# Optimization experiments

Measured on AMD Instinct MI355X. Metric: run time of the kernel, lower is better.

## Reference

```python
import jax, jax.numpy as jnp
import numpy as np

D_MODEL = 1024
NUM_HEADS = 16
D_K = D_MODEL // NUM_HEADS


def setup_inputs() -> dict:
    key = jax.random.key(0)
    k1, k2, k3 = jax.random.split(key, 3)
    x = jax.random.normal(k1, (2, 2048, D_MODEL), dtype=jnp.float32)
    # torch Linear(d, 3d): weight shape [3d, d], y = x @ W.T
    W_QKV = jax.random.normal(k2, (3 * D_MODEL, D_MODEL), dtype=jnp.float32) * (1.0 / np.sqrt(D_MODEL))
    W_O = jax.random.normal(k3, (D_MODEL, D_MODEL), dtype=jnp.float32) * (1.0 / np.sqrt(D_MODEL))
    return {"x": x, "W_QKV": W_QKV, "W_O": W_O}


def reference(x, W_QKV, W_O):
    B, T, C = x.shape
    qkv = jnp.einsum('btc,fc->btf', x, W_QKV)  # [B,T,3C]
    q, k, v = jnp.split(qkv, 3, axis=-1)
    def heads(t):
        return t.reshape(B, T, NUM_HEADS, D_K).transpose(0, 2, 1, 3)  # [B,H,T,Dk]
    Q, K, V = heads(q), heads(k), heads(v)
    scores = jnp.einsum('bhqd,bhkd->bhqk', Q, K) / jnp.sqrt(jnp.float32(D_K))
    causal = jnp.tril(jnp.ones((T, T), dtype=bool))
    scores = jnp.where(causal, scores, -jnp.inf)
    attn = jax.nn.softmax(scores, axis=-1)
    out = jnp.einsum('bhqk,bhkd->bhqd', attn, V)
    out = out.transpose(0, 2, 1, 3).reshape(B, T, C)
    return jnp.einsum('btc,oc->bto', out, W_O)
```

## Files before the change

kernel.cpp:

```cpp
#include <hip/hip_runtime.h>
#include <hip/hip_bf16.h>
#include <stdint.h>
#include <stddef.h>


typedef __attribute__((ext_vector_type(8)))  __bf16   bf16x8;
typedef __attribute__((ext_vector_type(4)))  float    f32x4;
typedef __attribute__((ext_vector_type(16))) float    f32x16;
typedef __attribute__((ext_vector_type(4)))  uint32_t u32x4;

#define AS1(p) ((__attribute__((address_space(1))) void*)(p))
#define AS3(p) ((__attribute__((address_space(3))) void*)(p))

static constexpr int Tq    = 2048;
static constexpr int Cd    = 1024;
static constexpr int Mrows = 2 * Tq;

#define QSCALE 0.18033688011112042f

__global__ __launch_bounds__(256) void cvt_bf16_kernel(const float* __restrict__ in,
                                                       __bf16* __restrict__ out, int n8)
{
    int idx    = blockIdx.x * blockDim.x + threadIdx.x;
    int stride = gridDim.x * blockDim.x;
    for (int i = idx; i < n8; i += stride) {
        f32x4 a = ((const f32x4*)in)[i * 2 + 0];
        f32x4 b = ((const f32x4*)in)[i * 2 + 1];
        bf16x8 o;
#pragma unroll
        for (int j = 0; j < 4; ++j) { o[j] = (__bf16)a[j]; o[4 + j] = (__bf16)b[j]; }
        ((bf16x8*)out)[i] = o;
    }
}

__global__ __launch_bounds__(256) void transpose_v_kernel(const __bf16* __restrict__ qkv,
                                                          __bf16* __restrict__ vT)
{
    __shared__ __bf16 tile[64][65];
    const int t   = threadIdx.x;
    const int r0  = blockIdx.x * 64;
    const int hd0 = blockIdx.y * 64;

    {
        const int rr = t >> 2, c16 = (t & 3) * 16;
        const __bf16* src = qkv + (size_t)(r0 + rr) * 3072 + 2048 + hd0 + c16;
        bf16x8 a = *(const bf16x8*)(src);
        bf16x8 b = *(const bf16x8*)(src + 8);
#pragma unroll
        for (int j = 0; j < 8; ++j) { tile[rr][c16 + j] = a[j]; tile[rr][c16 + 8 + j] = b[j]; }
    }
    __syncthreads();
    {
        const int hd_loc = t >> 2, rg = (t & 3) * 16;
        bf16x8 a, b;
#pragma unroll
        for (int j = 0; j < 8; ++j) { a[j] = tile[rg + j][hd_loc]; b[j] = tile[rg + 8 + j][hd_loc]; }
        __bf16* dst = vT + (size_t)(hd0 + hd_loc) * Mrows + r0 + rg;
        *(bf16x8*)(dst)     = a;
        *(bf16x8*)(dst + 8) = b;
    }
}

template <bool OUT_BF16>
__global__ __launch_bounds__(256) void gemm_bt_kernel(const __bf16* __restrict__ A,
                                                      const __bf16* __restrict__ Bm,
                                                      float* __restrict__ Cf,
                                                      __bf16* __restrict__ Cb,
                                                      int N, int K, int qcols, float qscale)
{
    __shared__ __align__(16) __bf16 As[128 * 64];
    __shared__ __align__(16) __bf16 Bs[128 * 64];

    const int tid = threadIdx.x;
    const int l   = tid & 63;
    const int w   = tid >> 6;
    const int wr  = w >> 1, wc = w & 1;
    const int lo  = l & 15, hi = l >> 4;
    const int m0  = blockIdx.x * 128;
    const int n0  = blockIdx.y * 128;

    f32x4 acc[4][4] = {};

    for (int kk = 0; kk < K; kk += 64) {
#pragma unroll
        for (int i = 0; i < 4; ++i) {
            int s   = i * 256 + tid;
            int row = s >> 3;
            int gg  = (s & 7) ^ (row & 7);
            const __bf16* srcA = A  + (size_t)(m0 + row) * K + kk + gg * 8;
            const __bf16* srcB = Bm + (size_t)(n0 + row) * K + kk + gg * 8;
            __builtin_amdgcn_global_load_lds(AS1(srcA), AS3((char*)As + s * 16), 16, 0, 0);
            __builtin_amdgcn_global_load_lds(AS1(srcB), AS3((char*)Bs + s * 16), 16, 0, 0);
        }
        __syncthreads();

#pragma unroll
        for (int ks = 0; ks < 2; ++ks) {
            bf16x8 af[4], bfr[4];
#pragma unroll
            for (int m = 0; m < 4; ++m) {
                int row = wr * 64 + m * 16 + lo;
                int gl  = (ks * 4 + hi) ^ (row & 7);
                af[m] = *(const bf16x8*)((const char*)As + row * 128 + gl * 16);
            }
#pragma unroll
            for (int n = 0; n < 4; ++n) {
                int row = wc * 64 + n * 16 + lo;
                int gl  = (ks * 4 + hi) ^ (row & 7);
                bfr[n] = *(const bf16x8*)((const char*)Bs + row * 128 + gl * 16);
            }
#pragma unroll
            for (int m = 0; m < 4; ++m)
#pragma unroll
                for (int n = 0; n < 4; ++n)
                    acc[m][n] = __builtin_amdgcn_mfma_f32_16x16x32_bf16(af[m], bfr[n], acc[m][n], 0, 0, 0);
        }
        __syncthreads();
    }

#pragma unroll
    for (int m = 0; m < 4; ++m)
#pragma unroll
        for (int n = 0; n < 4; ++n)
#pragma unroll
            for (int r = 0; r < 4; ++r) {
                int row = m0 + wr * 64 + m * 16 + hi * 4 + r;
                int col = n0 + wc * 64 + n * 16 + lo;
                float v = acc[m][n][r];
                if (col < qcols) v *= qscale;
                if (OUT_BF16) Cb[(size_t)row * N + col] = (__bf16)v;
                else          Cf[(size_t)row * N + col] = v;
            }
}

__global__ __launch_bounds__(128) void attn_kernel(const __bf16* __restrict__ qkv,
                                                   const __bf16* __restrict__ vT,
                                                   __bf16* __restrict__ att)
{
    __shared__ __align__(16) __bf16 Ks[2][64 * 64];
    __shared__ __align__(16) __bf16 Vs[2][64 * 64];

    const int tid = threadIdx.x;
    const int l   = tid & 63;
    const int w   = tid >> 6;
    const int lo5 = l & 31, hi5 = l >> 5;

    const int bid = blockIdx.x;
    const int g   = (bid >> 5) & 7;
    const int c   = bid >> 8;
    const int qt  = (c & 1) ? (16 - ((c >> 1) << 4) + g)
                            : (31 - ((c >> 1) << 4) - g);
    const int bh  = bid & 31;
    const int h   = bh & 15;
    const int b   = bh >> 4;

    const __bf16* Kbase = qkv + (size_t)b * Tq * 3072 + 1024 + h * 64;
    const __bf16* Vbase = vT  + (size_t)h * 64 * Mrows + b * Tq;

    const int qb0 = qt * 64;
    const int nt  = qt + 1;

    bf16x8 onesf;
#pragma unroll
    for (int jj = 0; jj < 8; ++jj) onesf[jj] = (__bf16)1.0f;

    bf16x8 qf[4];
    {
        const __bf16* Qp = qkv + (size_t)(b * Tq + qb0 + w * 32 + lo5) * 3072 + h * 64 + hi5 * 8;
#pragma unroll
        for (int ds = 0; ds < 4; ++ds) qf[ds] = *(const bf16x8*)(Qp + ds * 16);
    }

    f32x16 o0 = {}, o1 = {}, ls = {};
    float m = -1e30f;

#pragma unroll
    for (int i = 0; i < 4; ++i) {
        int s = i * 128 + tid;
        int row = s >> 3, gg = (s & 7) ^ (row & 7);
        __builtin_amdgcn_global_load_lds(AS1(Kbase + (size_t)row * 3072 + gg * 8),
                                         AS3((char*)Ks[0] + s * 16), 16, 0, 0);
        __builtin_amdgcn_global_load_lds(AS1(Vbase + (size_t)row * Mrows + gg * 8),
                                         AS3((char*)Vs[0] + s * 16), 16, 0, 0);
    }
    __syncthreads();

    int cur = 0;
    for (int t = 0; t < nt; ++t) {
        if (t + 1 < nt) {
            const int kn = (t + 1) * 64;
#pragma unroll
            for (int i = 0; i < 4; ++i) {
                int s = i * 128 + tid;
                int row = s >> 3, gg = (s & 7) ^ (row & 7);
                __builtin_amdgcn_global_load_lds(AS1(Kbase + (size_t)(kn + row) * 3072 + gg * 8),
                                                 AS3((char*)Ks[cur ^ 1] + s * 16), 16, 0, 0);
                __builtin_amdgcn_global_load_lds(AS1(Vbase + (size_t)row * Mrows + kn + gg * 8),
                                                 AS3((char*)Vs[cur ^ 1] + s * 16), 16, 0, 0);
            }
        }

        f32x16 sf0 = {}, sf1 = {};
        __builtin_amdgcn_s_setprio(1);
#pragma unroll
        for (int ds = 0; ds < 4; ++ds) {
            {
                int row = lo5;
                int gl  = (ds * 2 + hi5) ^ (row & 7);
                bf16x8 kf = *(const bf16x8*)((const char*)Ks[cur] + row * 128 + gl * 16);
                sf0 = __builtin_amdgcn_mfma_f32_32x32x16_bf16(kf, qf[ds], sf0, 0, 0, 0);
            }
            {
                int row = 32 + lo5;
                int gl  = (ds * 2 + hi5) ^ (row & 7);
                bf16x8 kf = *(const bf16x8*)((const char*)Ks[cur] + row * 128 + gl * 16);
                sf1 = __builtin_amdgcn_mfma_f32_32x32x16_bf16(kf, qf[ds], sf1, 0, 0, 0);
            }
        }
        __builtin_amdgcn_s_setprio(0);

        if (t == qt) {
            const int ql = w * 32 + lo5;
#pragma unroll
            for (int r = 0; r < 16; ++r) {
                int kc = (r & 3) + 8 * (r >> 2) + 4 * hi5;
                if (kc      > ql) sf0[r] = -1e30f;
                if (kc + 32 > ql) sf1[r] = -1e30f;
            }
        }

        float t0 = fmaxf(sf0[0],  fmaxf(sf0[1],  sf0[2]));
        float t1 = fmaxf(sf0[3],  fmaxf(sf0[4],  sf0[5]));
        float t2 = fmaxf(sf0[6],  fmaxf(sf0[7],  sf0[8]));
        float t3 = fmaxf(sf0[9],  fmaxf(sf0[10], sf0[11]));
        float t4 = fmaxf(sf0[12], fmaxf(sf0[13], sf0[14]));
        float t5 = fmaxf(sf1[0],  fmaxf(sf1[1],  sf1[2]));
        float t6 = fmaxf(sf1[3],  fmaxf(sf1[4],  sf1[5]));
        float t7 = fmaxf(sf1[6],  fmaxf(sf1[7],  sf1[8]));
        float t8 = fmaxf(sf1[9],  fmaxf(sf1[10], sf1[11]));
        float t9 = fmaxf(sf1[12], fmaxf(sf1[13], sf1[14]));
        float u0 = fmaxf(t0, fmaxf(t1, t2));
        float u1 = fmaxf(t3, fmaxf(t4, sf0[15]));
        float u2 = fmaxf(t5, fmaxf(t6, t7));
        float u3 = fmaxf(t8, fmaxf(t9, sf1[15]));
        float pmh = fmaxf(fmaxf(u0, u1), fmaxf(u2, u3));
        float pm  = fmaxf(pmh, __shfl_xor(pmh, 32));

        if (__any(pm > m + 8.0f)) {
            float mnew = fmaxf(m, pm);
            float fac  = __builtin_amdgcn_exp2f(m - mnew);
            m = mnew;
#pragma unroll
            for (int r = 0; r < 16; ++r) {
                int qreg = (r & 3) + 8 * (r >> 2) + 4 * hi5;
                float fr = __shfl(fac, qreg);
                o0[r] *= fr;
                o1[r] *= fr;
                ls[r] *= fr;
            }
        }

        __builtin_amdgcn_s_setprio(1);
#pragma unroll
        for (int kb = 0; kb < 2; ++kb) {
            uint32_t W[8];
#pragma unroll
            for (int wd = 0; wd < 8; ++wd) {
                float sa = (kb == 0) ? sf0[2 * wd]     : sf1[2 * wd];
                float sb = (kb == 0) ? sf0[2 * wd + 1] : sf1[2 * wd + 1];
                __bf16 ba = (__bf16)__builtin_amdgcn_exp2f(sa - m);
                __bf16 bb = (__bf16)__builtin_amdgcn_exp2f(sb - m);
                W[wd] = (uint32_t)__builtin_bit_cast(uint16_t, ba)
                      | ((uint32_t)__builtin_bit_cast(uint16_t, bb) << 16);
            }
            uint32_t Za = __shfl_xor(hi5 ? W[0] : W[2], 32);
            uint32_t Zb = __shfl_xor(hi5 ? W[1] : W[3], 32);
            uint32_t Zc = __shfl_xor(hi5 ? W[4] : W[6], 32);
            uint32_t Zd = __shfl_xor(hi5 ? W[5] : W[7], 32);

            {
                u32x4 fw = { hi5 ? Za : W[0], hi5 ? Zb : W[1],
                             hi5 ? W[2] : Za, hi5 ? W[3] : Zb };
                bf16x8 pa = __builtin_bit_cast(bf16x8, fw);
                const int kstep = kb * 2;
                {
                    int row = lo5;
                    int gl  = (kstep * 2 + hi5) ^ (row & 7);
                    bf16x8 vb = *(const bf16x8*)((const char*)Vs[cur] + row * 128 + gl * 16);
                    o0 = __builtin_amdgcn_mfma_f32_32x32x16_bf16(pa, vb, o0, 0, 0, 0);
                }
                {
                    int row = 32 + lo5;
                    int gl  = (kstep * 2 + hi5) ^ (row & 7);
                    bf16x8 vb = *(const bf16x8*)((const char*)Vs[cur] + row * 128 + gl * 16);
                    o1 = __builtin_amdgcn_mfma_f32_32x32x16_bf16(pa, vb, o1, 0, 0, 0);
                }
                ls = __builtin_amdgcn_mfma_f32_32x32x16_bf16(pa, onesf, ls, 0, 0, 0);
            }
            {
                u32x4 fw = { hi5 ? Zc : W[4], hi5 ? Zd : W[5],
                             hi5 ? W[6] : Zc, hi5 ? W[7] : Zd };
                bf16x8 pa = __builtin_bit_cast(bf16x8, fw);
                const int kstep = kb * 2 + 1;
                {
                    int row = lo5;
                    int gl  = (kstep * 2 + hi5) ^ (row & 7);
                    bf16x8 vb = *(const bf16x8*)((const char*)Vs[cur] + row * 128 + gl * 16);
                    o0 = __builtin_amdgcn_mfma_f32_32x32x16_bf16(pa, vb, o0, 0, 0, 0);
                }
                {
                    int row = 32 + lo5;
                    int gl  = (kstep * 2 + hi5) ^ (row & 7);
                    bf16x8 vb = *(const bf16x8*)((const char*)Vs[cur] + row * 128 + gl * 16);
                    o1 = __builtin_amdgcn_mfma_f32_32x32x16_bf16(pa, vb, o1, 0, 0, 0);
                }
                ls = __builtin_amdgcn_mfma_f32_32x32x16_bf16(pa, onesf, ls, 0, 0, 0);
            }
        }
        __builtin_amdgcn_s_setprio(0);

        __syncthreads();
        cur ^= 1;
    }

#pragma unroll
    for (int r = 0; r < 16; ++r) {
        float lr   = __builtin_amdgcn_rcpf(ls[r]);
        int   qreg = (r & 3) + 8 * (r >> 2) + 4 * hi5;
        int   rowg = b * Tq + qb0 + w * 32 + qreg;
        att[(size_t)rowg * Cd + h * 64 + lo5]      = (__bf16)(o0[r] * lr);
        att[(size_t)rowg * Cd + h * 64 + 32 + lo5] = (__bf16)(o1[r] * lr);
    }
}

extern "C" void kernel_launch(void* const* d_in, const int* in_sizes, int n_in,
                              void* d_out, int out_size, void* d_ws, size_t ws_size,
                              hipStream_t stream)
{
    (void)in_sizes; (void)n_in; (void)out_size; (void)ws_size;

    const float* x    = (const float*)d_in[0];
    const float* Wqkv = (const float*)d_in[1];
    const float* Wo   = (const float*)d_in[2];
    float*       out  = (float*)d_out;

    char* ws = (char*)d_ws;
    __bf16* xb    = (__bf16*)(ws);
    __bf16* wqkvb = (__bf16*)(ws + (size_t)8  * 1024 * 1024);
    __bf16* wob   = (__bf16*)(ws + (size_t)14 * 1024 * 1024);
    __bf16* qkvb  = (__bf16*)(ws + (size_t)16 * 1024 * 1024);
    __bf16* attb  = (__bf16*)(ws + (size_t)40 * 1024 * 1024);
    __bf16* vTb   = xb;

    cvt_bf16_kernel<<<2048, 256, 0, stream>>>(x,    xb,    Mrows * Cd / 8);
    cvt_bf16_kernel<<<1536, 256, 0, stream>>>(Wqkv, wqkvb, 3 * Cd * Cd / 8);
    cvt_bf16_kernel<<<512,  256, 0, stream>>>(Wo,   wob,   Cd * Cd / 8);

    dim3 g1(Mrows / 128, 3 * Cd / 128);
    gemm_bt_kernel<true><<<g1, 256, 0, stream>>>(xb, wqkvb, nullptr, qkvb, 3 * Cd, Cd,
                                                 1024, QSCALE);

    dim3 gt(Mrows / 64, Cd / 64);
    transpose_v_kernel<<<gt, 256, 0, stream>>>(qkvb, vTb);

    attn_kernel<<<1024, 128, 0, stream>>>(qkvb, vTb, attb);

    dim3 g2(Mrows / 128, Cd / 128);
    gemm_bt_kernel<false><<<g2, 256, 0, stream>>>(attb, wob, out, nullptr, Cd, Cd,
                                                  0, 1.0f);
}
```

Measured before the change: 206.2 us.

## Split long causal attention rows into KV chunks with a merge kernel

Query tiles 16-31, which have the longest causal KV ranges, are split into two KV chunks processed by separate blocks. Each chunk writes its unnormalized partial output and its running max and sum to scratch, reusing the output buffer and the freed weight buffer. A new merge kernel combines the two partials. Short tiles still go straight to the output. This targets load imbalance in the tail of the attention grid, at the cost of an extra launch and fp32 partial traffic.

```diff
diff --git a/kernel.cpp b/kernel.cpp
--- a/kernel.cpp
+++ b/kernel.cpp
@@ -133,10 +133,19 @@
             }
 }
 
-__global__ __launch_bounds__(128) void attn_kernel(const __bf16* __restrict__ qkv,
-                                                   const __bf16* __restrict__ vT,
-                                                   __bf16* __restrict__ att)
-{
+__global__ __launch_bounds__(128) void attn_chunk_kernel(const __bf16* __restrict__ qkv,
+                                                         const __bf16* __restrict__ vT,
+                                                         __bf16* __restrict__ att,
+                                                         float* __restrict__ pO,
+                                                         float* __restrict__ stats)
+{
+    constexpr uint8_t QT[48] = {16,17,18,19,20,21,22,23,24,25,26,27,28,29,30,31,
+                                15,31,14,30,13,29,12,28,11,27,10,26, 9,25, 8,24,
+                                 7,23, 6,22, 5,21, 4,20, 3,19, 2,18, 1,17, 0,16};
+    constexpr uint8_t CC[48] = {0,0,0,0,0,0,0,0,0,0,0,0,0,0,0,0,
+                                255,1,255,1,255,1,255,1,255,1,255,1,255,1,255,1,
+                                255,1,255,1,255,1,255,1,255,1,255,1,255,1,255,1};
+
     __shared__ __align__(16) __bf16 Ks[2][64 * 64];
     __shared__ __align__(16) __bf16 Vs[2][64 * 64];
 
@@ -146,19 +155,20 @@
     const int lo5 = l & 31, hi5 = l >> 5;
 
     const int bid = blockIdx.x;
-    const int g   = (bid >> 5) & 7;
-    const int c   = bid >> 8;
-    const int qt  = (c & 1) ? (16 - ((c >> 1) << 4) + g)
-                            : (31 - ((c >> 1) << 4) - g);
+    const int ord = bid >> 5;
     const int bh  = bid & 31;
     const int h   = bh & 15;
     const int b   = bh >> 4;
 
+    const int  qt     = QT[ord];
+    const int  cc     = CC[ord];
+    const bool direct = (cc == 255);
+    const int  t0     = direct ? 0 : cc * 16;
+    const int  t1     = direct ? qt + 1 : min(cc * 16 + 16, qt + 1);
+    const int  qb0    = qt * 64;
+
     const __bf16* Kbase = qkv + (size_t)b * Tq * 3072 + 1024 + h * 64;
     const __bf16* Vbase = vT  + (size_t)h * 64 * Mrows + b * Tq;
-
-    const int qb0 = qt * 64;
-    const int nt  = qt + 1;
 
     bf16x8 onesf;
 #pragma unroll
@@ -178,16 +188,16 @@
     for (int i = 0; i < 4; ++i) {
         int s = i * 128 + tid;
         int row = s >> 3, gg = (s & 7) ^ (row & 7);
-        __builtin_amdgcn_global_load_lds(AS1(Kbase + (size_t)row * 3072 + gg * 8),
+        __builtin_amdgcn_global_load_lds(AS1(Kbase + (size_t)(t0 * 64 + row) * 3072 + gg * 8),
                                          AS3((char*)Ks[0] + s * 16), 16, 0, 0);
-        __builtin_amdgcn_global_load_lds(AS1(Vbase + (size_t)row * Mrows + gg * 8),
+        __builtin_amdgcn_global_load_lds(AS1(Vbase + (size_t)row * Mrows + t0 * 64 + gg * 8),
                                          AS3((char*)Vs[0] + s * 16), 16, 0, 0);
     }
     __syncthreads();
 
     int cur = 0;
-    for (int t = 0; t < nt; ++t) {
-        if (t + 1 < nt) {
+    for (int t = t0; t < t1; ++t) {
+        if (t + 1 < t1) {
             const int kn = (t + 1) * 64;
 #pragma unroll
             for (int i = 0; i < 4; ++i) {
@@ -229,20 +239,20 @@
             }
         }
 
-        float t0 = fmaxf(sf0[0],  fmaxf(sf0[1],  sf0[2]));
-        float t1 = fmaxf(sf0[3],  fmaxf(sf0[4],  sf0[5]));
-        float t2 = fmaxf(sf0[6],  fmaxf(sf0[7],  sf0[8]));
-        float t3 = fmaxf(sf0[9],  fmaxf(sf0[10], sf0[11]));
-        float t4 = fmaxf(sf0[12], fmaxf(sf0[13], sf0[14]));
-        float t5 = fmaxf(sf1[0],  fmaxf(sf1[1],  sf1[2]));
-        float t6 = fmaxf(sf1[3],  fmaxf(sf1[4],  sf1[5]));
-        float t7 = fmaxf(sf1[6],  fmaxf(sf1[7],  sf1[8]));
-        float t8 = fmaxf(sf1[9],  fmaxf(sf1[10], sf1[11]));
-        float t9 = fmaxf(sf1[12], fmaxf(sf1[13], sf1[14]));
-        float u0 = fmaxf(t0, fmaxf(t1, t2));
-        float u1 = fmaxf(t3, fmaxf(t4, sf0[15]));
-        float u2 = fmaxf(t5, fmaxf(t6, t7));
-        float u3 = fmaxf(t8, fmaxf(t9, sf1[15]));
+        float t0m = fmaxf(sf0[0],  fmaxf(sf0[1],  sf0[2]));
+        float t1m = fmaxf(sf0[3],  fmaxf(sf0[4],  sf0[5]));
+        float t2m = fmaxf(sf0[6],  fmaxf(sf0[7],  sf0[8]));
+        float t3m = fmaxf(sf0[9],  fmaxf(sf0[10], sf0[11]));
+        float t4m = fmaxf(sf0[12], fmaxf(sf0[13], sf0[14]));
+        float t5m = fmaxf(sf1[0],  fmaxf(sf1[1],  sf1[2]));
+        float t6m = fmaxf(sf1[3],  fmaxf(sf1[4],  sf1[5]));
+        float t7m = fmaxf(sf1[6],  fmaxf(sf1[7],  sf1[8]));
+        float t8m = fmaxf(sf1[9],  fmaxf(sf1[10], sf1[11]));
+        float t9m = fmaxf(sf1[12], fmaxf(sf1[13], sf1[14]));
+        float u0 = fmaxf(t0m, fmaxf(t1m, t2m));
+        float u1 = fmaxf(t3m, fmaxf(t4m, sf0[15]));
+        float u2 = fmaxf(t5m, fmaxf(t6m, t7m));
+        float u3 = fmaxf(t8m, fmaxf(t9m, sf1[15]));
         float pmh = fmaxf(fmaxf(u0, u1), fmaxf(u2, u3));
         float pm  = fmaxf(pmh, __shfl_xor(pmh, 32));
 
@@ -323,14 +333,75 @@
         cur ^= 1;
     }
 
-#pragma unroll
-    for (int r = 0; r < 16; ++r) {
-        float lr   = __builtin_amdgcn_rcpf(ls[r]);
-        int   qreg = (r & 3) + 8 * (r >> 2) + 4 * hi5;
-        int   rowg = b * Tq + qb0 + w * 32 + qreg;
-        att[(size_t)rowg * Cd + h * 64 + lo5]      = (__bf16)(o0[r] * lr);
-        att[(size_t)rowg * Cd + h * 64 + 32 + lo5] = (__bf16)(o1[r] * lr);
-    }
+    if (direct) {
+#pragma unroll
+        for (int r = 0; r < 16; ++r) {
+            float lr   = __builtin_amdgcn_rcpf(ls[r]);
+            int   qreg = (r & 3) + 8 * (r >> 2) + 4 * hi5;
+            int   rowg = b * Tq + qb0 + w * 32 + qreg;
+            att[(size_t)rowg * Cd + h * 64 + lo5]      = (__bf16)(o0[r] * lr);
+            att[(size_t)rowg * Cd + h * 64 + 32 + lo5] = (__bf16)(o1[r] * lr);
+        }
+    } else {
+        const int slot = bh * 32 + (qt - 16) * 2 + cc;
+        float* po = pO + (size_t)slot * 4096;
+#pragma unroll
+        for (int r = 0; r < 16; ++r) {
+            int   qreg = (r & 3) + 8 * (r >> 2) + 4 * hi5;
+            int   row  = w * 32 + qreg;
+            po[row * 64 + lo5]      = o0[r];
+            po[row * 64 + 32 + lo5] = o1[r];
+            float mq = __shfl(m, qreg);
+            if (lo5 == 0) {
+                stats[(size_t)slot * 128 + row * 2 + 0] = mq;
+                stats[(size_t)slot * 128 + row * 2 + 1] = ls[r];
+            }
+        }
+    }
+}
+
+__global__ __launch_bounds__(256) void attn_merge_kernel(const float* __restrict__ pO,
+                                                         const float* __restrict__ stats,
+                                                         __bf16* __restrict__ att)
+{
+    const int mo  = blockIdx.x;
+    const int bh  = mo & 31;
+    const int qq  = mo >> 5;
+    const int qt  = 16 + qq;
+    const int h   = bh & 15;
+    const int b   = bh >> 4;
+
+    const int slot0 = bh * 32 + qq * 2;
+    const int slot1 = slot0 + 1;
+
+    const int tid = threadIdx.x;
+    const int row = tid >> 2;
+    const int c16 = (tid & 3) * 16;
+
+    float m0 = stats[(size_t)slot0 * 128 + row * 2 + 0];
+    float l0 = stats[(size_t)slot0 * 128 + row * 2 + 1];
+    float m1 = stats[(size_t)slot1 * 128 + row * 2 + 0];
+    float l1 = stats[(size_t)slot1 * 128 + row * 2 + 1];
+    float M  = fmaxf(m0, m1);
+    float w0 = exp2f(m0 - M);
+    float w1 = exp2f(m1 - M);
+    float inv = 1.0f / (w0 * l0 + w1 * l1);
+
+    const float* p0 = pO + (size_t)slot0 * 4096 + row * 64 + c16;
+    const float* p1 = pO + (size_t)slot1 * 4096 + row * 64 + c16;
+
+    bf16x8 ov[2];
+#pragma unroll
+    for (int i = 0; i < 4; ++i) {
+        f32x4 a = ((const f32x4*)p0)[i];
+        f32x4 bb = ((const f32x4*)p1)[i];
+#pragma unroll
+        for (int j = 0; j < 4; ++j)
+            ov[i >> 1][(i & 1) * 4 + j] = (__bf16)((w0 * a[j] + w1 * bb[j]) * inv);
+    }
+    __bf16* dst = att + (size_t)(b * Tq + qt * 64 + row) * Cd + h * 64 + c16;
+    *(bf16x8*)(dst)     = ov[0];
+    *(bf16x8*)(dst + 8) = ov[1];
 }
 
 extern "C" void kernel_launch(void* const* d_in, const int* in_sizes, int n_in,
@@ -351,6 +422,8 @@
     __bf16* qkvb  = (__bf16*)(ws + (size_t)16 * 1024 * 1024);
     __bf16* attb  = (__bf16*)(ws + (size_t)40 * 1024 * 1024);
     __bf16* vTb   = xb;
+    float*  stats = (float*)wqkvb;
+    float*  pO    = out;
 
     cvt_bf16_kernel<<<2048, 256, 0, stream>>>(x,    xb,    Mrows * Cd / 8);
     cvt_bf16_kernel<<<1536, 256, 0, stream>>>(Wqkv, wqkvb, 3 * Cd * Cd / 8);
@@ -363,7 +436,8 @@
     dim3 gt(Mrows / 64, Cd / 64);
     transpose_v_kernel<<<gt, 256, 0, stream>>>(qkvb, vTb);
 
-    attn_kernel<<<1024, 128, 0, stream>>>(qkvb, vTb, attb);
+    attn_chunk_kernel<<<1536, 128, 0, stream>>>(qkvb, vTb, attb, pO, stats);
+    attn_merge_kernel<<<512, 256, 0, stream>>>(pO, stats, attb);
 
     dim3 g2(Mrows / 128, Cd / 128);
     gemm_bt_kernel<false><<<g2, 256, 0, stream>>>(attb, wob, out, nullptr, Cd, Cd,
```

After: 208.6 us. About the same (+1.2%).
